# Kernel tuning notes

Hardware: AMD Instinct MI355X
Metric: run time of the kernel (lower is better)

## Reference

```python
import jax, jax.numpy as jnp
import numpy as np

H = 16       # num heads
HD = 64      # head dim
D = H * HD   # hidden size

def _rotate_half(x):
    x1, x2 = jnp.split(x, 2, axis=-1)
    return jnp.concatenate([-x2, x1], axis=-1)

def setup_inputs() -> dict:
    key = jax.random.key(0)
    ks = jax.random.split(key, 12)
    B, N, NP = 16, 1029, 1024  # batch, tokens (5 prefix + 1024 patches), patch tokens
    inp = {
        "hidden_states": jax.random.normal(ks[0], (B, N, D), dtype=jnp.float32),
        "sin": jax.random.uniform(ks[1], (NP, HD), dtype=jnp.float32, minval=-1.0, maxval=1.0),
        "cos": jax.random.uniform(ks[2], (NP, HD), dtype=jnp.float32, minval=-1.0, maxval=1.0),
        "Wq": jax.random.normal(ks[3], (D, D), dtype=jnp.float32) * 0.02,
        "bq": jnp.zeros((D,), dtype=jnp.float32),
        "Wk": jax.random.normal(ks[4], (D, D), dtype=jnp.float32) * 0.02,
        "bk": jnp.zeros((D,), dtype=jnp.float32),
        "Wv": jax.random.normal(ks[5], (D, D), dtype=jnp.float32) * 0.02,
        "bv": jnp.zeros((D,), dtype=jnp.float32),
        "Wo": jax.random.normal(ks[6], (D, D), dtype=jnp.float32) * 0.02,
        "bo": jnp.zeros((D,), dtype=jnp.float32),
    }
    return inp

def reference(hidden_states, sin, cos, Wq, bq, Wk, bk, Wv, bv, Wo, bo):
    B, N, _ = hidden_states.shape
    scaling = HD ** -0.5
    # qkv projections (nn.Linear: x @ W.T + b), split to heads: [B,H,N,HD]
    def proj(W, b):
        y = hidden_states @ W.T + b
        return y.reshape(B, N, H, HD).transpose(0, 2, 1, 3)
    q, k, v = proj(Wq, bq), proj(Wk, bk), proj(Wv, bv)
    # rotary pos emb on patch-token suffix only
    prefix = N - sin.shape[-2]
    def rope(x):
        xs = x[:, :, prefix:, :]
        xs = xs * cos + _rotate_half(xs) * sin
        return jnp.concatenate([x[:, :, :prefix, :], xs], axis=2)
    q, k = rope(q), rope(k)
    # eager attention: softmax in fp32
    attn = jnp.einsum("bhqd,bhkd->bhqk", q, k) * scaling
    attn = jax.nn.softmax(attn.astype(jnp.float32), axis=-1).astype(q.dtype)
    out = jnp.einsum("bhqk,bhkd->bhqd", attn, v)
    out = out.transpose(0, 2, 1, 3).reshape(B, N, D)
    return out @ Wo.T + bo
```

## Files before the change

### kernel.cpp

```cpp
#include <hip/hip_runtime.h>
#include <stdint.h>

#define H 16
#define HD 64
#define D 1024
#define NTOK 1029
#define BATCH 16
#define NPAD 1152
#define M_ROWS (BATCH*NTOK)
#define MPAD 16640
#define MT256 65
#define KB 1024
#define PREFIX 5

typedef unsigned short u16;
typedef __attribute__((ext_vector_type(8))) short short8;
typedef __attribute__((ext_vector_type(4))) short short4v;
typedef __attribute__((ext_vector_type(4))) float float4v;
typedef __attribute__((ext_vector_type(4))) unsigned int uint4v;

__device__ __forceinline__ u16 f2bf(float x) {
  unsigned int u = __float_as_uint(x);
  u += 0x7FFFu + ((u >> 16) & 1u);
  return (u16)(u >> 16);
}

__device__ __forceinline__ void gload16(const void* g, void* l) {
  __builtin_amdgcn_global_load_lds((const __attribute__((address_space(1))) void*)g,
                                   (__attribute__((address_space(3))) void*)l, 16, 0, 0);
}

__global__ __launch_bounds__(256) void cvt_A_kernel(const float* __restrict__ src,
                                                    u16* __restrict__ dst) {
  int idx = blockIdx.x * 256 + threadIdx.x;
  int m = idx >> 8, k = (idx & 255) * 4;
  float4v x = (float4v)0.f;
  if (m < M_ROWS) x = *(const float4v*)(src + (size_t)m * D + k);
  short4v o;
#pragma unroll
  for (int j = 0; j < 4; j++) o[j] = (short)f2bf(x[j]);
  *(short4v*)(dst + (size_t)m * D + k) = o;
}

__global__ __launch_bounds__(256) void cvt_W_kernel(
    const float* __restrict__ w0, const float* __restrict__ w1,
    const float* __restrict__ w2, const float* __restrict__ w3,
    u16* __restrict__ e0, u16* __restrict__ e1, u16* __restrict__ e2, u16* __restrict__ e3) {
  const float* src = (blockIdx.y == 0) ? w0 : (blockIdx.y == 1) ? w1 : (blockIdx.y == 2) ? w2 : w3;
  u16* dst = (blockIdx.y == 0) ? e0 : (blockIdx.y == 1) ? e1 : (blockIdx.y == 2) ? e2 : e3;
  int idx = blockIdx.x * 256 + threadIdx.x;
  int m = idx >> 8, k = (idx & 255) * 4;
  float4v x = *(const float4v*)(src + (size_t)m * D + k);
  short4v o;
#pragma unroll
  for (int j = 0; j < 4; j++) o[j] = (short)f2bf(x[j]);
  *(short4v*)(dst + (size_t)m * D + k) = o;
}


__device__ __forceinline__ void stage256(const u16* __restrict__ gA, const u16* __restrict__ gB,
                                         u16* dA, u16* dB, int dwo) {
#pragma unroll
  for (int i = 0; i < 4; i++)
    gload16(gA + (size_t)i * 64 * KB, dA + i * 4096 + dwo);
#pragma unroll
  for (int i = 0; i < 4; i++)
    gload16(gB + (size_t)i * 64 * KB, dB + i * 4096 + dwo);
}

#define GPHASE(mh, soffv, loadB)                                                          \
  {                                                                                       \
    short8 afr[4];                                                                        \
    _Pragma("unroll") for (int m4 = 0; m4 < 4; m4++)                                      \
        afr[m4] = *(const short8*)(pA + (wm_idx * 128 + ((mh)*4 + m4) * 16 + ar) * 64 + (soffv)); \
    if (loadB) {                                                                          \
      _Pragma("unroll") for (int ns = 0; ns < 4; ns++)                                    \
          bfr[ns] = *(const short8*)(pB + (wn_idx * 64 + ns * 16 + ar) * 64 + (soffv));   \
    }                                                                                     \
    __builtin_amdgcn_s_barrier();                                                         \
    asm volatile("s_waitcnt lgkmcnt(0)" ::: "memory");                                    \
    __builtin_amdgcn_s_setprio(1);                                                        \
    _Pragma("unroll") for (int m4 = 0; m4 < 4; m4++) {                                    \
      _Pragma("unroll") for (int ns = 0; ns < 4; ns++)                                    \
        acc[(mh)*4 + m4][ns] = __builtin_amdgcn_mfma_f32_16x16x32_bf16(                   \
            afr[m4], bfr[ns], acc[(mh)*4 + m4][ns], 0, 0, 0);                             \
    }                                                                                     \
    __builtin_amdgcn_s_setprio(0);                                                        \
    __builtin_amdgcn_s_barrier();                                                         \
  }

__device__ __forceinline__ void gemm256_mainloop(const u16* __restrict__ A,
                                                 const u16* __restrict__ Bw,
                                                 u16 As[2][16384], u16 Bs[2][16384],
                                                 int mtile, int ntile, float4v acc[8][4]) {
  const int tid = threadIdx.x;
  const int lane = tid & 63;
  const int wave = tid >> 6;
  const int wm_idx = wave >> 2;
  const int wn_idx = wave & 3;
  const int ar = lane & 15;
  const int kq = lane >> 4;
  const int s0 = ((kq)     ^ (ar & 7)) * 8;
  const int s1 = ((4 + kq) ^ (ar & 7)) * 8;
  const int srow = tid >> 3;
  const int scol = ((tid & 7) ^ (srow & 7)) * 8;
  const int dwo = (tid & ~63) * 8;
  const size_t abase = (size_t)mtile * 256 * KB + (size_t)srow * KB + scol;
  const size_t bbase = (size_t)ntile * 256 * KB + (size_t)srow * KB + scol;

#pragma unroll
  for (int i = 0; i < 8; i++)
#pragma unroll
    for (int j = 0; j < 4; j++) acc[i][j] = (float4v)0.f;

  stage256(A + abase, Bw + bbase, As[0], Bs[0], dwo);
  stage256(A + abase + 64, Bw + bbase + 64, As[1], Bs[1], dwo);
  asm volatile("s_waitcnt vmcnt(8)" ::: "memory");
  __builtin_amdgcn_s_barrier();

  short8 bfr[4];
  for (int t = 0; t < 16; ++t) {
    const u16* pA = As[t & 1];
    const u16* pB = Bs[t & 1];
    GPHASE(0, s0, 1)
    GPHASE(1, s0, 0)
    GPHASE(0, s1, 1)
    GPHASE(1, s1, 0)
    if (t < 14) {
      const int k0 = (t + 2) * 64;
      stage256(A + abase + k0, Bw + bbase + k0, As[t & 1], Bs[t & 1], dwo);
      asm volatile("s_waitcnt vmcnt(8)" ::: "memory");
    } else {
      asm volatile("s_waitcnt vmcnt(0)" ::: "memory");
    }
    __builtin_amdgcn_s_barrier();
  }
}

__global__ __launch_bounds__(512, 2) void gemm_qkv_kernel(
    const u16* __restrict__ A,
    const u16* __restrict__ Wqb, const u16* __restrict__ Wkb, const u16* __restrict__ Wvb,
    const float* __restrict__ bq, const float* __restrict__ bk, const float* __restrict__ bv,
    const float* __restrict__ sinp, const float* __restrict__ cosp,
    u16* __restrict__ qb, u16* __restrict__ kb, u16* __restrict__ vt) {
  __shared__ __align__(16) u16 As[2][16384];
  __shared__ __align__(16) u16 Bs[2][16384];
  const int z = blockIdx.z;
  const u16* Bw = (z == 0) ? Wqb : (z == 1) ? Wkb : Wvb;
  const float* bias = (z == 0) ? bq : (z == 1) ? bk : bv;
  const int ntile = blockIdx.x, mtile = blockIdx.y;
  float4v acc[8][4];
  gemm256_mainloop(A, Bw, As, Bs, mtile, ntile, acc);

  const int tid = threadIdx.x, lane = tid & 63, wave = tid >> 6;
  const int wm_idx = wave >> 2, wn_idx = wave & 3;
  const int ar = lane & 15, kq = lane >> 4;
  const int rowb = mtile * 256 + wm_idx * 128;
  const int colb = ntile * 256 + wn_idx * 64;
#pragma unroll
  for (int ms = 0; ms < 8; ms++) {
#pragma unroll
    for (int r = 0; r < 4; r++) {
      int grow = rowb + ms * 16 + kq * 4 + r;
      if (grow >= M_ROWS) continue;
      int b = grow / NTOK;
      int n = grow - b * NTOK;
      bool dorope = (z != 2) && (n >= PREFIX);
      int pos = n - PREFIX;
#pragma unroll
      for (int ns = 0; ns < 4; ns++) {
        int col = colb + ns * 16 + ar;
        int hh = col >> 6, d = col & 63;
        float y = acc[ms][ns][r] + bias[col];
        if (z == 2) {
          vt[((size_t)(b * H + hh) * 64 + d) * NPAD + n] = f2bf(y);
          continue;
        }
        if (dorope) {
          float xp = acc[ms][ns ^ 2][r] + bias[col ^ 32];
          float c = cosp[pos * HD + d], s = sinp[pos * HD + d];
          y = y * c + ((d < 32) ? -xp : xp) * s;
        }
        if (z == 0) y *= 0.125f;
        u16* outp = (z == 0) ? qb : kb;
        outp[((size_t)(b * H + hh) * NPAD + n) * 64 + d] = f2bf(y);
      }
    }
  }
}

#define SSHIFT 3.0f
#define NJT 17
__global__ __launch_bounds__(256) void attn_kernel(const u16* __restrict__ qb,
                                                   const u16* __restrict__ kb,
                                                   const u16* __restrict__ vt,
                                                   u16* __restrict__ ao) {
  __shared__ __align__(16) u16 sQ[128 * 72];
  __shared__ __align__(16) u16 sK[64 * 72];
  __shared__ __align__(16) u16 sV[64 * 72];
  const int tid = threadIdx.x, lane = tid & 63, wave = tid >> 6;
  const int ar = lane & 15, kq = lane >> 4;
  const int qt = blockIdx.x, hh = blockIdx.y, b = blockIdx.z;
  const int bh = b * H + hh;
  const u16* qbase = qb + (size_t)bh * NPAD * 64;
  const u16* kbase = kb + (size_t)bh * NPAD * 64;
  const u16* vbase = vt + (size_t)bh * 64 * NPAD;

#pragma unroll
  for (int i = 0; i < 4; i++) {
    int chunk = i * 256 + tid;
    int row = chunk >> 3, c = chunk & 7;
    *(uint4v*)(sQ + row * 72 + c * 8) =
        *(const uint4v*)(qbase + (size_t)(qt * 128 + row) * 64 + c * 8);
  }
  __syncthreads();
  short8 aq[2][2];
#pragma unroll
  for (int ms = 0; ms < 2; ms++)
#pragma unroll
    for (int ki = 0; ki < 2; ki++)
      aq[ms][ki] = *(const short8*)(sQ + (wave * 32 + ms * 16 + ar) * 72 + ki * 32 + kq * 8);
  u16* sP = sQ + wave * 32 * 72;

  float rs[2][4];
  float4v o_acc[2][4];
#pragma unroll
  for (int ms = 0; ms < 2; ms++)
#pragma unroll
    for (int r = 0; r < 4; r++) rs[ms][r] = 0.f;
#pragma unroll
  for (int ms = 0; ms < 2; ms++)
#pragma unroll
    for (int t = 0; t < 4; t++) o_acc[ms][t] = (float4v)0.f;

  for (int jt = 0; jt < NJT; jt++) {
    __syncthreads();
#pragma unroll
    for (int i = 0; i < 2; i++) {
      int chunk = i * 256 + tid;
      int row = chunk >> 3, c = chunk & 7;
      *(uint4v*)(sK + row * 72 + c * 8) =
          *(const uint4v*)(kbase + (size_t)(jt * 64 + row) * 64 + c * 8);
      *(uint4v*)(sV + row * 72 + c * 8) =
          *(const uint4v*)(vbase + (size_t)row * NPAD + jt * 64 + c * 8);
    }
    __syncthreads();

    float4v s[2][4];
#pragma unroll
    for (int ms = 0; ms < 2; ms++)
#pragma unroll
      for (int t = 0; t < 4; t++) s[ms][t] = (float4v)0.f;
#pragma unroll
    for (int ki = 0; ki < 2; ki++) {
#pragma unroll
      for (int t = 0; t < 4; t++) {
        short8 bk8 = *(const short8*)(sK + (t * 16 + ar) * 72 + ki * 32 + kq * 8);
#pragma unroll
        for (int ms = 0; ms < 2; ms++)
          s[ms][t] = __builtin_amdgcn_mfma_f32_16x16x32_bf16(aq[ms][ki], bk8, s[ms][t], 0, 0, 0);
      }
    }
    if (jt == NJT - 1) {
#pragma unroll
      for (int t = 0; t < 4; t++)
        if ((NJT - 1) * 64 + t * 16 + ar >= NTOK) {
#pragma unroll
          for (int ms = 0; ms < 2; ms++) s[ms][t] = (float4v)(-INFINITY);
        }
    }
    asm volatile("" ::: "memory");
#pragma unroll
    for (int ms = 0; ms < 2; ms++)
#pragma unroll
      for (int t = 0; t < 4; t++)
#pragma unroll
        for (int r = 0; r < 4; r++) {
          float p = __expf(s[ms][t][r] - SSHIFT);
          rs[ms][r] += p;
          sP[(ms * 16 + kq * 4 + r) * 72 + t * 16 + ar] = f2bf(p);
        }
    asm volatile("" ::: "memory");
#pragma unroll
    for (int ki = 0; ki < 2; ki++) {
#pragma unroll
      for (int ms = 0; ms < 2; ms++) {
        short8 ap = *(const short8*)(sP + (ms * 16 + ar) * 72 + ki * 32 + kq * 8);
#pragma unroll
        for (int t = 0; t < 4; t++) {
          short8 bv8 = *(const short8*)(sV + (t * 16 + ar) * 72 + ki * 32 + kq * 8);
          o_acc[ms][t] = __builtin_amdgcn_mfma_f32_16x16x32_bf16(ap, bv8, o_acc[ms][t], 0, 0, 0);
        }
      }
    }
  }
#pragma unroll
  for (int ms = 0; ms < 2; ms++)
#pragma unroll
    for (int r = 0; r < 4; r++) {
      float l = rs[ms][r];
#pragma unroll
      for (int off = 1; off < 16; off <<= 1) l += __shfl_xor(l, off, 64);
      int i = qt * 128 + wave * 32 + ms * 16 + kq * 4 + r;
      if (i >= NTOK) continue;
      float inv = 1.f / l;
      size_t mg = (size_t)b * NTOK + i;
#pragma unroll
      for (int t = 0; t < 4; t++)
        ao[mg * D + hh * 64 + t * 16 + ar] = f2bf(o_acc[ms][t][r] * inv);
    }
}

__global__ __launch_bounds__(512, 2) void gemm_o_kernel(const u16* __restrict__ A,
                                                        const u16* __restrict__ Wob,
                                                        const float* __restrict__ bo,
                                                        float* __restrict__ out) {
  __shared__ __align__(16) u16 As[2][16384];
  __shared__ __align__(16) u16 Bs[2][16384];
  const int ntile = blockIdx.x, mtile = blockIdx.y;
  float4v acc[8][4];
  gemm256_mainloop(A, Wob, As, Bs, mtile, ntile, acc);
  const int tid = threadIdx.x, lane = tid & 63, wave = tid >> 6;
  const int wm_idx = wave >> 2, wn_idx = wave & 3;
  const int ar = lane & 15, kq = lane >> 4;
  const int rowb = mtile * 256 + wm_idx * 128;
  const int colb = ntile * 256 + wn_idx * 64;
#pragma unroll
  for (int ms = 0; ms < 8; ms++) {
#pragma unroll
    for (int r = 0; r < 4; r++) {
      int grow = rowb + ms * 16 + kq * 4 + r;
      if (grow >= M_ROWS) continue;
#pragma unroll
      for (int ns = 0; ns < 4; ns++) {
        int col = colb + ns * 16 + ar;
        out[(size_t)grow * D + col] = acc[ms][ns][r] + bo[col];
      }
    }
  }
}

extern "C" void kernel_launch(void* const* d_in, const int* in_sizes, int n_in,
                              void* d_out, int out_size, void* d_ws, size_t ws_size,
                              hipStream_t stream) {
  const float* hidden = (const float*)d_in[0];
  const float* sinp = (const float*)d_in[1];
  const float* cosp = (const float*)d_in[2];
  const float* Wq = (const float*)d_in[3]; const float* bq = (const float*)d_in[4];
  const float* Wk = (const float*)d_in[5]; const float* bk = (const float*)d_in[6];
  const float* Wv = (const float*)d_in[7]; const float* bv = (const float*)d_in[8];
  const float* Wo = (const float*)d_in[9]; const float* bo = (const float*)d_in[10];
  float* out = (float*)d_out;
  (void)in_sizes; (void)n_in; (void)out_size; (void)ws_size;

  char* ws = (char*)d_ws;
  size_t off = 0;
  auto carve = [&](size_t elems) {
    u16* p = (u16*)(ws + off);
    off += ((elems * 2 + 255) & ~(size_t)255);
    return p;
  };
  u16* A_bf = carve((size_t)MPAD * KB);
  u16* Wqb = carve((size_t)D * KB);
  u16* Wkb = carve((size_t)D * KB);
  u16* Wvb = carve((size_t)D * KB);
  u16* Wob = carve((size_t)D * KB);
  u16* q_b = carve((size_t)BATCH * H * NPAD * 64);
  u16* k_b = carve((size_t)BATCH * H * NPAD * 64);
  u16* v_t = carve((size_t)BATCH * H * NPAD * 64);

  hipLaunchKernelGGL(cvt_A_kernel, dim3(MPAD), dim3(256), 0, stream, hidden, A_bf);
  hipLaunchKernelGGL(cvt_W_kernel, dim3(1024, 4), dim3(256), 0, stream,
                     Wq, Wk, Wv, Wo, Wqb, Wkb, Wvb, Wob);
  hipLaunchKernelGGL(gemm_qkv_kernel, dim3(4, MT256, 3), dim3(512), 0, stream,
                     A_bf, Wqb, Wkb, Wvb, bq, bk, bv, sinp, cosp, q_b, k_b, v_t);
  hipLaunchKernelGGL(attn_kernel, dim3(9, H, BATCH), dim3(256), 0, stream, q_b, k_b, v_t, A_bf);
  hipLaunchKernelGGL(gemm_o_kernel, dim3(4, MT256), dim3(512), 0, stream, A_bf, Wob, bo, out);
}
```

Before: 694.8 us.

## Interleave GEMM global-to-LDS staging across MFMA phases with fine-grained waits

```diff
diff --git a/kernel.cpp b/kernel.cpp
--- a/kernel.cpp
+++ b/kernel.cpp
@@ -58,25 +58,22 @@
 }
 
 
-__device__ __forceinline__ void stage256(const u16* __restrict__ gA, const u16* __restrict__ gB,
-                                         u16* dA, u16* dB, int dwo) {
-#pragma unroll
-  for (int i = 0; i < 4; i++)
-    gload16(gA + (size_t)i * 64 * KB, dA + i * 4096 + dwo);
-#pragma unroll
-  for (int i = 0; i < 4; i++)
-    gload16(gB + (size_t)i * 64 * KB, dB + i * 4096 + dwo);
-}
-
-#define GPHASE(mh, soffv, loadB)                                                          \
+#define STG(dst, src)                          \
+  do {                                         \
+    gload16((src), (dst) + dswo);              \
+    gload16((src) + 64 * KB, (dst) + 4096 + dswo); \
+  } while (0)
+
+#define GPHASE(mh, soffv, loadB, pA, pB, ...)                                             \
   {                                                                                       \
     short8 afr[4];                                                                        \
     _Pragma("unroll") for (int m4 = 0; m4 < 4; m4++)                                      \
-        afr[m4] = *(const short8*)(pA + (wm_idx * 128 + ((mh)*4 + m4) * 16 + ar) * 64 + (soffv)); \
+        afr[m4] = *(const short8*)((pA) + (wm_idx * 128 + ((mh)*4 + m4) * 16 + ar) * 64 + (soffv)); \
     if (loadB) {                                                                          \
       _Pragma("unroll") for (int ns = 0; ns < 4; ns++)                                    \
-          bfr[ns] = *(const short8*)(pB + (wn_idx * 64 + ns * 16 + ar) * 64 + (soffv));   \
+          bfr[ns] = *(const short8*)((pB) + (wn_idx * 64 + ns * 16 + ar) * 64 + (soffv)); \
     }                                                                                     \
+    __VA_ARGS__                                                                           \
     __builtin_amdgcn_s_barrier();                                                         \
     asm volatile("s_waitcnt lgkmcnt(0)" ::: "memory");                                    \
     __builtin_amdgcn_s_setprio(1);                                                        \
@@ -89,9 +86,22 @@
     __builtin_amdgcn_s_barrier();                                                         \
   }
 
+#define TILE(pA, pB, oA, oB, n1, S1, n2, S2)                                         \
+  GPHASE(0, s0, 1, pA, pB, if (S1) STG((oA) + 8192, Ab + 128 * KB + (size_t)(n1) * 64);) \
+  GPHASE(1, s0, 0, pA, pB, if (S1) STG((oB), Bb + (size_t)(n1) * 64);)               \
+  GPHASE(0, s1, 1, pA, pB, if (S1) STG((oB) + 8192, Bb + 128 * KB + (size_t)(n1) * 64);) \
+  GPHASE(1, s1, 0, pA, pB, )                                                         \
+  if (S2) {                                                                          \
+    STG((pA), Ab + (size_t)(n2) * 64);                                               \
+    asm volatile("s_waitcnt vmcnt(2)" ::: "memory");                                 \
+  } else {                                                                           \
+    asm volatile("s_waitcnt vmcnt(0)" ::: "memory");                                 \
+  }                                                                                  \
+  __builtin_amdgcn_s_barrier();
+
 __device__ __forceinline__ void gemm256_mainloop(const u16* __restrict__ A,
                                                  const u16* __restrict__ Bw,
-                                                 u16 As[2][16384], u16 Bs[2][16384],
+                                                 u16* As0, u16* Bs0, u16* As1, u16* Bs1,
                                                  int mtile, int ntile, float4v acc[8][4]) {
   const int tid = threadIdx.x;
   const int lane = tid & 63;
@@ -104,37 +114,31 @@
   const int s1 = ((4 + kq) ^ (ar & 7)) * 8;
   const int srow = tid >> 3;
   const int scol = ((tid & 7) ^ (srow & 7)) * 8;
-  const int dwo = (tid & ~63) * 8;
-  const size_t abase = (size_t)mtile * 256 * KB + (size_t)srow * KB + scol;
-  const size_t bbase = (size_t)ntile * 256 * KB + (size_t)srow * KB + scol;
+  const int dswo = (tid & ~63) * 8;
+  const u16* Ab = A + (size_t)mtile * 256 * KB + (size_t)srow * KB + scol;
+  const u16* Bb = Bw + (size_t)ntile * 256 * KB + (size_t)srow * KB + scol;
 
 #pragma unroll
   for (int i = 0; i < 8; i++)
 #pragma unroll
     for (int j = 0; j < 4; j++) acc[i][j] = (float4v)0.f;
 
-  stage256(A + abase, Bw + bbase, As[0], Bs[0], dwo);
-  stage256(A + abase + 64, Bw + bbase + 64, As[1], Bs[1], dwo);
-  asm volatile("s_waitcnt vmcnt(8)" ::: "memory");
+  STG(As0, Ab);
+  STG(As0 + 8192, Ab + 128 * KB);
+  STG(Bs0, Bb);
+  STG(Bs0 + 8192, Bb + 128 * KB);
+  STG(As1, Ab + 64);
+  asm volatile("s_waitcnt vmcnt(2)" ::: "memory");
   __builtin_amdgcn_s_barrier();
 
   short8 bfr[4];
-  for (int t = 0; t < 16; ++t) {
-    const u16* pA = As[t & 1];
-    const u16* pB = Bs[t & 1];
-    GPHASE(0, s0, 1)
-    GPHASE(1, s0, 0)
-    GPHASE(0, s1, 1)
-    GPHASE(1, s1, 0)
-    if (t < 14) {
-      const int k0 = (t + 2) * 64;
-      stage256(A + abase + k0, Bw + bbase + k0, As[t & 1], Bs[t & 1], dwo);
-      asm volatile("s_waitcnt vmcnt(8)" ::: "memory");
-    } else {
-      asm volatile("s_waitcnt vmcnt(0)" ::: "memory");
-    }
-    __builtin_amdgcn_s_barrier();
-  }
+#pragma unroll 1
+  for (int t2 = 0; t2 < 14; t2 += 2) {
+    TILE(As0, Bs0, As1, Bs1, t2 + 1, 1, t2 + 2, 1)
+    TILE(As1, Bs1, As0, Bs0, t2 + 2, 1, t2 + 3, 1)
+  }
+  TILE(As0, Bs0, As1, Bs1, 15, 1, 0, 0)
+  TILE(As1, Bs1, As0, Bs0, 0, 0, 0, 0)
 }
 
 __global__ __launch_bounds__(512, 2) void gemm_qkv_kernel(
@@ -143,14 +147,16 @@
     const float* __restrict__ bq, const float* __restrict__ bk, const float* __restrict__ bv,
     const float* __restrict__ sinp, const float* __restrict__ cosp,
     u16* __restrict__ qb, u16* __restrict__ kb, u16* __restrict__ vt) {
-  __shared__ __align__(16) u16 As[2][16384];
-  __shared__ __align__(16) u16 Bs[2][16384];
+  __shared__ __align__(16) u16 As0[16384];
+  __shared__ __align__(16) u16 Bs0[16384];
+  __shared__ __align__(16) u16 As1[16384];
+  __shared__ __align__(16) u16 Bs1[16384];
   const int z = blockIdx.z;
   const u16* Bw = (z == 0) ? Wqb : (z == 1) ? Wkb : Wvb;
   const float* bias = (z == 0) ? bq : (z == 1) ? bk : bv;
   const int ntile = blockIdx.x, mtile = blockIdx.y;
   float4v acc[8][4];
-  gemm256_mainloop(A, Bw, As, Bs, mtile, ntile, acc);
+  gemm256_mainloop(A, Bw, As0, Bs0, As1, Bs1, mtile, ntile, acc);
 
   const int tid = threadIdx.x, lane = tid & 63, wave = tid >> 6;
   const int wm_idx = wave >> 2, wn_idx = wave & 3;
@@ -315,11 +321,13 @@
                                                         const u16* __restrict__ Wob,
                                                         const float* __restrict__ bo,
                                                         float* __restrict__ out) {
-  __shared__ __align__(16) u16 As[2][16384];
-  __shared__ __align__(16) u16 Bs[2][16384];
+  __shared__ __align__(16) u16 As0[16384];
+  __shared__ __align__(16) u16 Bs0[16384];
+  __shared__ __align__(16) u16 As1[16384];
+  __shared__ __align__(16) u16 Bs1[16384];
   const int ntile = blockIdx.x, mtile = blockIdx.y;
   float4v acc[8][4];
-  gemm256_mainloop(A, Wob, As, Bs, mtile, ntile, acc);
+  gemm256_mainloop(A, Wob, As0, Bs0, As1, Bs1, mtile, ntile, acc);
   const int tid = threadIdx.x, lane = tid & 63, wave = tid >> 6;
   const int wm_idx = wave >> 2, wn_idx = wave & 3;
   const int ar = lane & 15, kq = lane >> 4;
```

Measured after the change: 655.5 us. 5.7% less time.
